# Kernel optimization log

Measured on AMD Instinct MI355X. Metric: run time of the kernel, lower is better.

The kernel has to match this reference:

```python
import jax, jax.numpy as jnp
import numpy as np

T = 300  # windowsize = windowstep(50) * windowmul(6)
D_IN = 39
H1, H2 = 35, 30
FC1, FC2, OUT = 50, 40, 2


def _lstm_layer(x_tbd, W, b, H):
    """TF LSTMCell: gates ordered i, j, f, o; forget_bias=1.0; tanh activation.
    x_tbd: [T, B, D]; W: [D+H, 4H]; b: [4H]. Returns hidden states [T, B, H]."""
    B = x_tbd.shape[1]
    h0 = jnp.zeros((B, H), x_tbd.dtype)
    c0 = jnp.zeros((B, H), x_tbd.dtype)

    def step(carry, xt):
        h, c = carry
        z = jnp.concatenate([xt, h], axis=-1) @ W + b  # [B, 4H]
        i, j, f, o = jnp.split(z, 4, axis=-1)
        c = jax.nn.sigmoid(f + 1.0) * c + jax.nn.sigmoid(i) * jnp.tanh(j)
        h = jax.nn.sigmoid(o) * jnp.tanh(c)
        return (h, c), h

    _, hs = jax.lax.scan(step, (h0, c0), x_tbd)
    return hs


def _stack(x_tbd, W1, b1, W2, b2):
    h1 = _lstm_layer(x_tbd, W1, b1, H1)
    return _lstm_layer(h1, W2, b2, H2)


def setup_inputs() -> dict:
    key = jax.random.key(0)
    ks = jax.random.split(key, 16)
    B = 4096
    s = lambda fan_in: 1.0 / np.sqrt(fan_in)

    def mat(k, shape):
        return jax.random.normal(k, shape, jnp.float32) * s(shape[0])

    return {
        "x": jax.random.normal(ks[0], (B, T, D_IN), jnp.float32),
        "fw_W1": mat(ks[1], (D_IN + H1, 4 * H1)), "fw_b1": jnp.zeros((4 * H1,), jnp.float32),
        "fw_W2": mat(ks[2], (H1 + H2, 4 * H2)), "fw_b2": jnp.zeros((4 * H2,), jnp.float32),
        "bw_W1": mat(ks[3], (D_IN + H1, 4 * H1)), "bw_b1": jnp.zeros((4 * H1,), jnp.float32),
        "bw_W2": mat(ks[4], (H1 + H2, 4 * H2)), "bw_b2": jnp.zeros((4 * H2,), jnp.float32),
        "W_fc1": mat(ks[5], (2 * H2, FC1)), "b_fc1": jnp.zeros((FC1,), jnp.float32),
        "W_fc2": mat(ks[6], (FC1, FC2)), "b_fc2": jnp.zeros((FC2,), jnp.float32),
        "W_out": mat(ks[7], (FC2, OUT)), "b_out": jnp.zeros((OUT,), jnp.float32),
    }


def reference(x, fw_W1, fw_b1, fw_W2, fw_b2, bw_W1, bw_b1, bw_W2, bw_b2,
              W_fc1, b_fc1, W_fc2, b_fc2, W_out, b_out):
    x_tbd = jnp.transpose(x, (1, 0, 2))  # [T, B, D]
    h_fw = _stack(x_tbd, fw_W1, fw_b1, fw_W2, fw_b2)               # [T, B, H2]
    h_bw = _stack(x_tbd[::-1], bw_W1, bw_b1, bw_W2, bw_b2)[::-1]   # [T, B, H2]
    h = jnp.concatenate([h_fw, h_bw], axis=-1)  # [T, B, 2*H2]
    h = jnp.transpose(h, (1, 0, 2))             # [B, T, 60]
    h = jax.nn.relu(h @ W_fc1 + b_fc1)
    h = jax.nn.relu(h @ W_fc2 + b_fc2)
    logits = h @ W_out + b_out                  # [B, T, 2]
    return logits
```

## Files before the change

kernel.cpp:

```cpp
#include <hip/hip_runtime.h>


#define T_STEPS 300
#define DIN 39
#define H1 35
#define H2 30
#define BATCH 4096
#define FC1N 50
#define FC2N 40

#define AP_STR 104

typedef _Float16 f16;
typedef _Float16 half8 __attribute__((ext_vector_type(8)));
typedef float floatx4 __attribute__((ext_vector_type(4)));

__device__ __forceinline__ float sigf(float x) {
    return __builtin_amdgcn_rcpf(1.0f + __expf(-x));
}
__device__ __forceinline__ float sig_tanh(float a, float b) {
    float ea = __expf(-a);
    float E  = __expf(2.0f * b);
    return (E - 1.0f) * __builtin_amdgcn_rcpf((1.0f + ea) * (E + 1.0f));
}

__global__ void wprep_kernel(const float* __restrict__ fw1, const float* __restrict__ bw1,
                             const float* __restrict__ fw2, const float* __restrict__ bw2,
                             f16* __restrict__ bp) {
    int frag = blockIdx.x;
    int lane = threadIdx.x;
    int dir = frag / 60;
    int rem = frag % 60;
    int layer = (rem < 36) ? 0 : 1;
    int r2 = (layer == 0) ? rem : rem - 36;
    int ug = r2 / 12, g = (r2 % 12) / 3, c = r2 % 3;
    int u = ug * 16 + (lane & 15);
    const float* W = (layer == 0) ? (dir ? bw1 : fw1) : (dir ? bw2 : fw2);
    for (int j = 0; j < 8; ++j) {
        int k = c * 32 + (lane >> 4) * 8 + j;
        float v = 0.0f;
        if (layer == 0) {
            if (u < H1) {
                int kr = (k < 39) ? k : ((k >= 40 && k < 75) ? k - 1 : -1);
                if (kr >= 0) v = W[kr * (4 * H1) + g * H1 + u];
            }
        } else {
            if (u < H2 && k < 65) v = W[k * (4 * H2) + g * H2 + u];
        }
        bp[(size_t)frag * 512 + lane * 8 + j] = (f16)v;
    }
}

__global__ void fcwprep_kernel(const float* __restrict__ Wf1, const float* __restrict__ Wf2,
                               const float* __restrict__ Wo, f16* __restrict__ fcp) {
    int f = blockIdx.x;
    int lane = threadIdx.x;
    int lm = lane & 15, oct = lane >> 4;
    for (int j = 0; j < 8; ++j) {
        float v = 0.0f;
        if (f < 8) {
            int tile = f >> 1, chunk = f & 1;
            int n = tile * 16 + lm;
            int kl = chunk * 32 + oct * 8 + j;
            int krow = (kl < 30) ? kl : ((kl >= 32 && kl < 62) ? kl - 2 : -1);
            if (n < FC1N && krow >= 0) v = Wf1[krow * FC1N + n];
        } else if (f < 14) {
            int g = f - 8, tile = g >> 1, chunk = g & 1;
            int n = tile * 16 + lm;
            int k = chunk * 32 + oct * 8 + j;
            if (n < FC2N && k < FC1N) v = Wf2[k * FC2N + n];
        } else {
            int chunk = f - 14;
            int k = chunk * 32 + oct * 8 + j;
            if (lm < 2 && k < FC2N) v = Wo[k * 2 + lm];
        }
        fcp[(size_t)f * 512 + lane * 8 + j] = (f16)v;
    }
}

__global__ __launch_bounds__(320, 3) void lstm_fused(
    const float* __restrict__ x, const f16* __restrict__ bp,
    const float* __restrict__ fb1, const float* __restrict__ bb1,
    const float* __restrict__ fb2, const float* __restrict__ bb2,
    f16* __restrict__ h2s)
{
    __shared__ f16 pan1[2][16 * AP_STR];
    __shared__ f16 pan2[2][16 * AP_STR];

    const int tid = threadIdx.x;
    const int b0  = blockIdx.x * 16;
    const int dir = blockIdx.y;
    const int wv   = tid >> 6;
    const int lane = tid & 63;
    const int lm = lane & 15, oct = lane >> 4;
    const bool isL2 = (wv >= 3);
    const int ug = isL2 ? (wv - 3) : wv;
    const int u  = ug * 16 + lm;
    const int Hn = isL2 ? H2 : H1;
    const float* bias = isL2 ? (dir ? bb2 : fb2) : (dir ? bb1 : fb1);
    const int fragbase = dir * 60 + (isL2 ? 36 : 0) + ug * 12;

    half8 bf[4][3];
    #pragma unroll
    for (int g = 0; g < 4; ++g)
        #pragma unroll
        for (int c = 0; c < 3; ++c)
            bf[g][c] = *(const half8*)(bp + (size_t)(fragbase + g * 3 + c) * 512 + lane * 8);

    float zb[4];
    #pragma unroll
    for (int g = 0; g < 4; ++g)
        zb[g] = (u < Hn) ? bias[g * Hn + u] : 0.f;
    float cst[4] = {0.f, 0.f, 0.f, 0.f};

    for (int idx = tid; idx < 16 * AP_STR; idx += 320) {
        pan1[0][idx] = (f16)0.f; pan1[1][idx] = (f16)0.f;
        pan2[0][idx] = (f16)0.f; pan2[1][idx] = (f16)0.f;
    }
    __syncthreads();

    const int sr = tid / 10, sq = tid % 10;
    float xv[4] = {0.f, 0.f, 0.f, 0.f};
    if (tid < 160) {
        int t0 = dir ? (T_STEPS - 1) : 0;
        const float* p0 = x + ((size_t)(b0 + sr) * T_STEPS + t0) * DIN;
        union { f16 h[4]; uint2 u; } pk;
        #pragma unroll
        for (int i = 0; i < 4; ++i) { int k = sq * 4 + i; pk.h[i] = (k < DIN) ? (f16)p0[k] : (f16)0.f; }
        *(uint2*)(&pan1[0][sr * AP_STR + sq * 4]) = pk.u;
        int t1 = dir ? (T_STEPS - 2) : 1;
        const float* p1 = x + ((size_t)(b0 + sr) * T_STEPS + t1) * DIN;
        #pragma unroll
        for (int i = 0; i < 4; ++i) { int k = sq * 4 + i; xv[i] = (k < DIN) ? p1[k] : 0.f; }
    }
    __syncthreads();

    const int arow = lm * AP_STR + oct * 8;

    if (!isL2) {
        floatx4 C[4];
        #pragma unroll
        for (int g = 0; g < 4; ++g) C[g] = (floatx4){zb[g], zb[g], zb[g], zb[g]};
        half8 a0 = *(const half8*)(&pan1[0][arow]);
        half8 a1 = *(const half8*)(&pan1[0][arow + 32]);
        half8 a2 = *(const half8*)(&pan1[0][arow + 64]);
        #pragma unroll
        for (int g = 0; g < 4; ++g) {
            C[g] = __builtin_amdgcn_mfma_f32_16x16x32_f16(a0, bf[g][0], C[g], 0, 0, 0);
            C[g] = __builtin_amdgcn_mfma_f32_16x16x32_f16(a1, bf[g][1], C[g], 0, 0, 0);
            C[g] = __builtin_amdgcn_mfma_f32_16x16x32_f16(a2, bf[g][2], C[g], 0, 0, 0);
        }
        #pragma unroll
        for (int r = 0; r < 4; ++r) {
            float cc = sigf(C[2][r] + 1.0f) * cst[r] + sig_tanh(C[0][r], C[1][r]);
            cst[r] = cc;
            float hh = sig_tanh(C[3][r], cc);
            if (u < H1) {
                int row = oct * 4 + r;
                f16 hv = (f16)hh;
                pan1[1][row * AP_STR + 40 + u] = hv;
                pan2[1][row * AP_STR + u] = hv;
            }
        }
    }
    if (tid < 160) {
        union { f16 h[4]; uint2 u; } pk;
        #pragma unroll
        for (int i = 0; i < 4; ++i) pk.h[i] = (f16)xv[i];
        *(uint2*)(&pan1[1][sr * AP_STR + sq * 4]) = pk.u;
        int t2 = dir ? (T_STEPS - 3) : 2;
        const float* p2 = x + ((size_t)(b0 + sr) * T_STEPS + t2) * DIN;
        #pragma unroll
        for (int i = 0; i < 4; ++i) { int k = sq * 4 + i; xv[i] = (k < DIN) ? p2[k] : 0.f; }
    }
    __syncthreads();

    for (int s = 0; s < T_STEPS; ++s) {
        const int p = 1 - (s & 1);

        float xn[4] = {0.f, 0.f, 0.f, 0.f};
        if (tid < 160) {
            int sp = s + 3; if (sp > T_STEPS - 1) sp = T_STEPS - 1;
            int tp = dir ? (T_STEPS - 1 - sp) : sp;
            const float* px = x + ((size_t)(b0 + sr) * T_STEPS + tp) * DIN;
            #pragma unroll
            for (int i = 0; i < 4; ++i) { int k = sq * 4 + i; xn[i] = (k < DIN) ? px[k] : 0.f; }
        }

        const f16* ap = isL2 ? &pan2[p][0] : &pan1[p][0];
        half8 a0 = *(const half8*)(ap + arow);
        half8 a1 = *(const half8*)(ap + arow + 32);
        half8 a2 = *(const half8*)(ap + arow + 64);

        if (tid < 160) {
            union { f16 h[4]; uint2 u; } pk;
            #pragma unroll
            for (int i = 0; i < 4; ++i) pk.h[i] = (f16)xv[i];
            *(uint2*)(&pan1[1 - p][sr * AP_STR + sq * 4]) = pk.u;
            #pragma unroll
            for (int i = 0; i < 4; ++i) xv[i] = xn[i];
        }

        floatx4 C[4];
        #pragma unroll
        for (int g = 0; g < 4; ++g) C[g] = (floatx4){zb[g], zb[g], zb[g], zb[g]};
        #pragma unroll
        for (int g = 0; g < 4; ++g) {
            C[g] = __builtin_amdgcn_mfma_f32_16x16x32_f16(a0, bf[g][0], C[g], 0, 0, 0);
            C[g] = __builtin_amdgcn_mfma_f32_16x16x32_f16(a1, bf[g][1], C[g], 0, 0, 0);
            C[g] = __builtin_amdgcn_mfma_f32_16x16x32_f16(a2, bf[g][2], C[g], 0, 0, 0);
        }

        f16* w1 = &pan1[1 - p][0];
        f16* w2 = &pan2[1 - p][0];
        if (!isL2) {
            #pragma unroll
            for (int r = 0; r < 4; ++r) {
                float cc = sigf(C[2][r] + 1.0f) * cst[r] + sig_tanh(C[0][r], C[1][r]);
                cst[r] = cc;
                float hh = sig_tanh(C[3][r], cc);
                if (u < H1) {
                    int row = oct * 4 + r;
                    f16 hv = (f16)hh;
                    w1[row * AP_STR + 40 + u] = hv;
                    w2[row * AP_STR + u] = hv;
                }
            }
        } else {
            const int t_out = dir ? (T_STEPS - 1 - s) : s;
            #pragma unroll
            for (int r = 0; r < 4; ++r) {
                float dd = sigf(C[2][r] + 1.0f) * cst[r] + sig_tanh(C[0][r], C[1][r]);
                cst[r] = dd;
                float gg = sig_tanh(C[3][r], dd);
                if (u < H2) {
                    int row = oct * 4 + r;
                    f16 gv = (f16)gg;
                    w2[row * AP_STR + 35 + u] = gv;
                    h2s[((size_t)(dir * BATCH + b0 + row) * T_STEPS + t_out) * 32 + u] = gv;
                }
            }
        }

        __syncthreads();
    }
}

__global__ __launch_bounds__(256) void fc_kernel(
    const f16* __restrict__ h2s, const f16* __restrict__ fcp,
    const float* __restrict__ bf1, const float* __restrict__ bf2,
    const float* __restrict__ bo, float* __restrict__ out)
{
    __shared__ f16 apf[4][16 * 72];
    const int tid = threadIdx.x;
    const int wv = tid >> 6, lane = tid & 63;
    const int lm = lane & 15, oct = lane >> 4;
    f16* ap = apf[wv];

    half8 wf[16];
    #pragma unroll
    for (int f = 0; f < 16; ++f)
        wf[f] = *(const half8*)(fcp + (size_t)f * 512 + lane * 8);

    const int ar = lm * 72 + oct * 8;
    const int row = lane >> 2, seg = lane & 3;
    const size_t base = (size_t)blockIdx.x * 256 + wv * 64;

    uint4 vf = *(const uint4*)(h2s + (base + row) * 32 + seg * 8);
    uint4 vb = *(const uint4*)(h2s + ((size_t)BATCH * T_STEPS + base + row) * 32 + seg * 8);

    for (int it = 0; it < 4; ++it) {
        const size_t rid0 = base + it * 16;

        *(uint4*)(ap + row * 72 + seg * 8) = vf;
        *(uint4*)(ap + row * 72 + 32 + seg * 8) = vb;

        if (it < 3) {
            const size_t ridn = rid0 + 16;
            vf = *(const uint4*)(h2s + (ridn + row) * 32 + seg * 8);
            vb = *(const uint4*)(h2s + ((size_t)BATCH * T_STEPS + ridn + row) * 32 + seg * 8);
        }

        {
            half8 a0 = *(const half8*)(ap + ar);
            half8 a1 = *(const half8*)(ap + ar + 32);
            floatx4 C[4];
            #pragma unroll
            for (int t = 0; t < 4; ++t) {
                int col = t * 16 + lm;
                float b = (col < FC1N) ? bf1[col] : 0.f;
                C[t] = (floatx4){b, b, b, b};
                C[t] = __builtin_amdgcn_mfma_f32_16x16x32_f16(a0, wf[t * 2 + 0], C[t], 0, 0, 0);
                C[t] = __builtin_amdgcn_mfma_f32_16x16x32_f16(a1, wf[t * 2 + 1], C[t], 0, 0, 0);
            }
            #pragma unroll
            for (int t = 0; t < 4; ++t) {
                int col = t * 16 + lm;
                #pragma unroll
                for (int r = 0; r < 4; ++r)
                    ap[(oct * 4 + r) * 72 + col] = (f16)fmaxf(C[t][r], 0.f);
            }
        }
        {
            half8 a0 = *(const half8*)(ap + ar);
            half8 a1 = *(const half8*)(ap + ar + 32);
            floatx4 D[3];
            #pragma unroll
            for (int t = 0; t < 3; ++t) {
                int col = t * 16 + lm;
                float b = (col < FC2N) ? bf2[col] : 0.f;
                D[t] = (floatx4){b, b, b, b};
                D[t] = __builtin_amdgcn_mfma_f32_16x16x32_f16(a0, wf[8 + t * 2 + 0], D[t], 0, 0, 0);
                D[t] = __builtin_amdgcn_mfma_f32_16x16x32_f16(a1, wf[8 + t * 2 + 1], D[t], 0, 0, 0);
            }
            #pragma unroll
            for (int t = 0; t < 3; ++t) {
                int col = t * 16 + lm;
                #pragma unroll
                for (int r = 0; r < 4; ++r)
                    ap[(oct * 4 + r) * 72 + col] = (f16)fmaxf(D[t][r], 0.f);
            }
        }
        {
            half8 a0 = *(const half8*)(ap + ar);
            half8 a1 = *(const half8*)(ap + ar + 32);
            float b = (lm < 2) ? bo[lm] : 0.f;
            floatx4 E = (floatx4){b, b, b, b};
            E = __builtin_amdgcn_mfma_f32_16x16x32_f16(a0, wf[14], E, 0, 0, 0);
            E = __builtin_amdgcn_mfma_f32_16x16x32_f16(a1, wf[15], E, 0, 0, 0);
            if (lm < 2) {
                #pragma unroll
                for (int r = 0; r < 4; ++r)
                    out[(rid0 + oct * 4 + r) * 2 + lm] = E[r];
            }
        }
    }
}

extern "C" void kernel_launch(void* const* d_in, const int* in_sizes, int n_in,
                              void* d_out, int out_size, void* d_ws, size_t ws_size,
                              hipStream_t stream) {
    const float* x     = (const float*)d_in[0];
    const float* fw_W1 = (const float*)d_in[1];
    const float* fw_b1 = (const float*)d_in[2];
    const float* fw_W2 = (const float*)d_in[3];
    const float* fw_b2 = (const float*)d_in[4];
    const float* bw_W1 = (const float*)d_in[5];
    const float* bw_b1 = (const float*)d_in[6];
    const float* bw_W2 = (const float*)d_in[7];
    const float* bw_b2 = (const float*)d_in[8];
    const float* Wf1   = (const float*)d_in[9];
    const float* bf1   = (const float*)d_in[10];
    const float* Wf2   = (const float*)d_in[11];
    const float* bf2   = (const float*)d_in[12];
    const float* Wo    = (const float*)d_in[13];
    const float* bo    = (const float*)d_in[14];
    float* outp = (float*)d_out;

    f16* h2s = (f16*)d_ws;
    f16* bp  = h2s + (size_t)2 * BATCH * T_STEPS * 32;
    f16* fcp = bp + (size_t)120 * 512;

    wprep_kernel<<<120, 64, 0, stream>>>(fw_W1, bw_W1, fw_W2, bw_W2, bp);
    fcwprep_kernel<<<16, 64, 0, stream>>>(Wf1, Wf2, Wo, fcp);

    dim3 gl(BATCH / 16, 2);
    lstm_fused<<<gl, 320, 0, stream>>>(x, bp, fw_b1, bw_b1, fw_b2, bw_b2, h2s);

    fc_kernel<<<(BATCH * T_STEPS) / 256, 256, 0, stream>>>(
        h2s, fcp, bf1, bf2, bo, outp);
}
```

Before: 713.2 us.

## Restructure LSTM step pointers and x staging; batch FC kernel loads across row groups

In the recurrent kernel, the next-step x pointer and the h2 output pointer become running pointers instead of being recomputed each step. The x staging store into shared memory moves after the gate math, so the MFMA chain starts sooner, and tanh's exponent argument is clamped to avoid overflow. The FC kernel now loads all four 16-row groups up front into a larger shared buffer and processes each layer across all groups, with a launch-bounds occupancy hint. This aims to cut address arithmetic and expose more memory-level parallelism, at the cost of more shared memory and registers in the FC kernel.

```diff
diff --git a/kernel.cpp b/kernel.cpp
--- a/kernel.cpp
+++ b/kernel.cpp
@@ -19,8 +19,9 @@
     return __builtin_amdgcn_rcpf(1.0f + __expf(-x));
 }
 __device__ __forceinline__ float sig_tanh(float a, float b) {
+    float bc = fminf(b, 30.0f);
     float ea = __expf(-a);
-    float E  = __expf(2.0f * b);
+    float E  = __expf(2.0f * bc);
     return (E - 1.0f) * __builtin_amdgcn_rcpf((1.0f + ea) * (E + 1.0f));
 }
 
@@ -113,6 +114,10 @@
         zb[g] = (u < Hn) ? bias[g * Hn + u] : 0.f;
     float cst[4] = {0.f, 0.f, 0.f, 0.f};
 
+    f16* h2p = h2s + ((size_t)(dir * BATCH + b0 + oct * 4) * T_STEPS
+                      + (dir ? (T_STEPS - 1) : 0)) * 32 + u;
+    const int h2step = dir ? -32 : 32;
+
     for (int idx = tid; idx < 16 * AP_STR; idx += 320) {
         pan1[0][idx] = (f16)0.f; pan1[1][idx] = (f16)0.f;
         pan2[0][idx] = (f16)0.f; pan2[1][idx] = (f16)0.f;
@@ -163,6 +168,9 @@
             }
         }
     }
+    const float* px = x + ((size_t)(b0 + sr) * T_STEPS
+                           + (dir ? (T_STEPS - 4) : 3)) * DIN + sq * 4;
+    const int xstep = dir ? -DIN : DIN;
     if (tid < 160) {
         union { f16 h[4]; uint2 u; } pk;
         #pragma unroll
@@ -180,35 +188,25 @@
 
         float xn[4] = {0.f, 0.f, 0.f, 0.f};
         if (tid < 160) {
-            int sp = s + 3; if (sp > T_STEPS - 1) sp = T_STEPS - 1;
-            int tp = dir ? (T_STEPS - 1 - sp) : sp;
-            const float* px = x + ((size_t)(b0 + sr) * T_STEPS + tp) * DIN;
-            #pragma unroll
-            for (int i = 0; i < 4; ++i) { int k = sq * 4 + i; xn[i] = (k < DIN) ? px[k] : 0.f; }
-        }
+            #pragma unroll
+            for (int i = 0; i < 4; ++i) { int k = sq * 4 + i; xn[i] = (k < DIN) ? px[i] : 0.f; }
+        }
+        if (s < T_STEPS - 4) px += xstep;
 
         const f16* ap = isL2 ? &pan2[p][0] : &pan1[p][0];
-        half8 a0 = *(const half8*)(ap + arow);
-        half8 a1 = *(const half8*)(ap + arow + 32);
-        half8 a2 = *(const half8*)(ap + arow + 64);
-
-        if (tid < 160) {
-            union { f16 h[4]; uint2 u; } pk;
-            #pragma unroll
-            for (int i = 0; i < 4; ++i) pk.h[i] = (f16)xv[i];
-            *(uint2*)(&pan1[1 - p][sr * AP_STR + sq * 4]) = pk.u;
-            #pragma unroll
-            for (int i = 0; i < 4; ++i) xv[i] = xn[i];
-        }
-
         floatx4 C[4];
         #pragma unroll
         for (int g = 0; g < 4; ++g) C[g] = (floatx4){zb[g], zb[g], zb[g], zb[g]};
-        #pragma unroll
-        for (int g = 0; g < 4; ++g) {
-            C[g] = __builtin_amdgcn_mfma_f32_16x16x32_f16(a0, bf[g][0], C[g], 0, 0, 0);
-            C[g] = __builtin_amdgcn_mfma_f32_16x16x32_f16(a1, bf[g][1], C[g], 0, 0, 0);
-            C[g] = __builtin_amdgcn_mfma_f32_16x16x32_f16(a2, bf[g][2], C[g], 0, 0, 0);
+        {
+            half8 a0 = *(const half8*)(ap + arow);
+            half8 a1 = *(const half8*)(ap + arow + 32);
+            half8 a2 = *(const half8*)(ap + arow + 64);
+            #pragma unroll
+            for (int g = 0; g < 4; ++g) {
+                C[g] = __builtin_amdgcn_mfma_f32_16x16x32_f16(a0, bf[g][0], C[g], 0, 0, 0);
+                C[g] = __builtin_amdgcn_mfma_f32_16x16x32_f16(a1, bf[g][1], C[g], 0, 0, 0);
+                C[g] = __builtin_amdgcn_mfma_f32_16x16x32_f16(a2, bf[g][2], C[g], 0, 0, 0);
+            }
         }
 
         f16* w1 = &pan1[1 - p][0];
@@ -227,7 +225,6 @@
                 }
             }
         } else {
-            const int t_out = dir ? (T_STEPS - 1 - s) : s;
             #pragma unroll
             for (int r = 0; r < 4; ++r) {
                 float dd = sigf(C[2][r] + 1.0f) * cst[r] + sig_tanh(C[0][r], C[1][r]);
@@ -237,21 +234,30 @@
                     int row = oct * 4 + r;
                     f16 gv = (f16)gg;
                     w2[row * AP_STR + 35 + u] = gv;
-                    h2s[((size_t)(dir * BATCH + b0 + row) * T_STEPS + t_out) * 32 + u] = gv;
+                    h2p[(size_t)r * T_STEPS * 32] = gv;
                 }
             }
         }
-
+        h2p += h2step;
+
+        if (tid < 160) {
+            union { f16 h[4]; uint2 u; } pk;
+            #pragma unroll
+            for (int i = 0; i < 4; ++i) pk.h[i] = (f16)xv[i];
+            *(uint2*)(&pan1[1 - p][sr * AP_STR + sq * 4]) = pk.u;
+            #pragma unroll
+            for (int i = 0; i < 4; ++i) xv[i] = xn[i];
+        }
         __syncthreads();
     }
 }
 
-__global__ __launch_bounds__(256) void fc_kernel(
+__global__ __launch_bounds__(256, 4) void fc_kernel(
     const f16* __restrict__ h2s, const f16* __restrict__ fcp,
     const float* __restrict__ bf1, const float* __restrict__ bf2,
     const float* __restrict__ bo, float* __restrict__ out)
 {
-    __shared__ f16 apf[4][16 * 72];
+    __shared__ f16 apf[4][64 * 72];
     const int tid = threadIdx.x;
     const int wv = tid >> 6, lane = tid & 63;
     const int lm = lane & 15, oct = lane >> 4;
@@ -266,73 +272,79 @@
     const int row = lane >> 2, seg = lane & 3;
     const size_t base = (size_t)blockIdx.x * 256 + wv * 64;
 
-    uint4 vf = *(const uint4*)(h2s + (base + row) * 32 + seg * 8);
-    uint4 vb = *(const uint4*)(h2s + ((size_t)BATCH * T_STEPS + base + row) * 32 + seg * 8);
-
-    for (int it = 0; it < 4; ++it) {
-        const size_t rid0 = base + it * 16;
-
-        *(uint4*)(ap + row * 72 + seg * 8) = vf;
-        *(uint4*)(ap + row * 72 + 32 + seg * 8) = vb;
-
-        if (it < 3) {
-            const size_t ridn = rid0 + 16;
-            vf = *(const uint4*)(h2s + (ridn + row) * 32 + seg * 8);
-            vb = *(const uint4*)(h2s + ((size_t)BATCH * T_STEPS + ridn + row) * 32 + seg * 8);
-        }
-
-        {
-            half8 a0 = *(const half8*)(ap + ar);
-            half8 a1 = *(const half8*)(ap + ar + 32);
-            floatx4 C[4];
-            #pragma unroll
-            for (int t = 0; t < 4; ++t) {
-                int col = t * 16 + lm;
-                float b = (col < FC1N) ? bf1[col] : 0.f;
-                C[t] = (floatx4){b, b, b, b};
-                C[t] = __builtin_amdgcn_mfma_f32_16x16x32_f16(a0, wf[t * 2 + 0], C[t], 0, 0, 0);
-                C[t] = __builtin_amdgcn_mfma_f32_16x16x32_f16(a1, wf[t * 2 + 1], C[t], 0, 0, 0);
-            }
-            #pragma unroll
-            for (int t = 0; t < 4; ++t) {
-                int col = t * 16 + lm;
-                #pragma unroll
-                for (int r = 0; r < 4; ++r)
-                    ap[(oct * 4 + r) * 72 + col] = (f16)fmaxf(C[t][r], 0.f);
-            }
-        }
-        {
-            half8 a0 = *(const half8*)(ap + ar);
-            half8 a1 = *(const half8*)(ap + ar + 32);
-            floatx4 D[3];
-            #pragma unroll
-            for (int t = 0; t < 3; ++t) {
-                int col = t * 16 + lm;
-                float b = (col < FC2N) ? bf2[col] : 0.f;
-                D[t] = (floatx4){b, b, b, b};
-                D[t] = __builtin_amdgcn_mfma_f32_16x16x32_f16(a0, wf[8 + t * 2 + 0], D[t], 0, 0, 0);
-                D[t] = __builtin_amdgcn_mfma_f32_16x16x32_f16(a1, wf[8 + t * 2 + 1], D[t], 0, 0, 0);
-            }
-            #pragma unroll
-            for (int t = 0; t < 3; ++t) {
-                int col = t * 16 + lm;
-                #pragma unroll
-                for (int r = 0; r < 4; ++r)
-                    ap[(oct * 4 + r) * 72 + col] = (f16)fmaxf(D[t][r], 0.f);
-            }
-        }
-        {
-            half8 a0 = *(const half8*)(ap + ar);
-            half8 a1 = *(const half8*)(ap + ar + 32);
-            float b = (lm < 2) ? bo[lm] : 0.f;
-            floatx4 E = (floatx4){b, b, b, b};
-            E = __builtin_amdgcn_mfma_f32_16x16x32_f16(a0, wf[14], E, 0, 0, 0);
-            E = __builtin_amdgcn_mfma_f32_16x16x32_f16(a1, wf[15], E, 0, 0, 0);
-            if (lm < 2) {
-                #pragma unroll
-                for (int r = 0; r < 4; ++r)
-                    out[(rid0 + oct * 4 + r) * 2 + lm] = E[r];
-            }
+    uint4 vf[4], vb[4];
+    #pragma unroll
+    for (int g = 0; g < 4; ++g) {
+        const size_t r0 = base + g * 16 + row;
+        vf[g] = *(const uint4*)(h2s + r0 * 32 + seg * 8);
+        vb[g] = *(const uint4*)(h2s + ((size_t)BATCH * T_STEPS + r0) * 32 + seg * 8);
+    }
+    #pragma unroll
+    for (int g = 0; g < 4; ++g) {
+        *(uint4*)(ap + (g * 16 + row) * 72 + seg * 8) = vf[g];
+        *(uint4*)(ap + (g * 16 + row) * 72 + 32 + seg * 8) = vb[g];
+    }
+
+    #pragma unroll
+    for (int g = 0; g < 4; ++g) {
+        f16* agp = ap + g * 16 * 72;
+        half8 a0 = *(const half8*)(agp + ar);
+        half8 a1 = *(const half8*)(agp + ar + 32);
+        floatx4 C[4];
+        #pragma unroll
+        for (int t = 0; t < 4; ++t) {
+            int col = t * 16 + lm;
+            float b = (col < FC1N) ? bf1[col] : 0.f;
+            C[t] = (floatx4){b, b, b, b};
+            C[t] = __builtin_amdgcn_mfma_f32_16x16x32_f16(a0, wf[t * 2 + 0], C[t], 0, 0, 0);
+            C[t] = __builtin_amdgcn_mfma_f32_16x16x32_f16(a1, wf[t * 2 + 1], C[t], 0, 0, 0);
+        }
+        #pragma unroll
+        for (int t = 0; t < 4; ++t) {
+            int col = t * 16 + lm;
+            #pragma unroll
+            for (int r = 0; r < 4; ++r)
+                agp[(oct * 4 + r) * 72 + col] = (f16)fmaxf(C[t][r], 0.f);
+        }
+    }
+
+    #pragma unroll
+    for (int g = 0; g < 4; ++g) {
+        f16* agp = ap + g * 16 * 72;
+        half8 a0 = *(const half8*)(agp + ar);
+        half8 a1 = *(const half8*)(agp + ar + 32);
+        floatx4 D[3];
+        #pragma unroll
+        for (int t = 0; t < 3; ++t) {
+            int col = t * 16 + lm;
+            float b = (col < FC2N) ? bf2[col] : 0.f;
+            D[t] = (floatx4){b, b, b, b};
+            D[t] = __builtin_amdgcn_mfma_f32_16x16x32_f16(a0, wf[8 + t * 2 + 0], D[t], 0, 0, 0);
+            D[t] = __builtin_amdgcn_mfma_f32_16x16x32_f16(a1, wf[8 + t * 2 + 1], D[t], 0, 0, 0);
+        }
+        #pragma unroll
+        for (int t = 0; t < 3; ++t) {
+            int col = t * 16 + lm;
+            #pragma unroll
+            for (int r = 0; r < 4; ++r)
+                agp[(oct * 4 + r) * 72 + col] = (f16)fmaxf(D[t][r], 0.f);
+        }
+    }
+
+    #pragma unroll
+    for (int g = 0; g < 4; ++g) {
+        f16* agp = ap + g * 16 * 72;
+        half8 a0 = *(const half8*)(agp + ar);
+        half8 a1 = *(const half8*)(agp + ar + 32);
+        float b = (lm < 2) ? bo[lm] : 0.f;
+        floatx4 E = (floatx4){b, b, b, b};
+        E = __builtin_amdgcn_mfma_f32_16x16x32_f16(a0, wf[14], E, 0, 0, 0);
+        E = __builtin_amdgcn_mfma_f32_16x16x32_f16(a1, wf[15], E, 0, 0, 0);
+        if (lm < 2) {
+            const size_t rid0 = base + g * 16;
+            #pragma unroll
+            for (int r = 0; r < 4; ++r)
+                out[(rid0 + oct * 4 + r) * 2 + lm] = E[r];
         }
     }
 }
```

Result: faster. 665.9 us (-6.6%).
